# Kernel optimization log

Hardware: AMD Instinct MI355X
Metric: run time of the kernel (lower is better)

## Reference

```python
import jax, jax.numpy as jnp
import numpy as np

N = 100000   # nodes
DEG = 16     # fixed neighbor count per node
F_IN = 128
F_OUT = 32
H = 4        # heads


def setup_inputs() -> dict:
    key = jax.random.key(0)
    k1, k2, k3, k4 = jax.random.split(key, 4)
    x = jax.random.normal(k1, (N, F_IN), dtype=jnp.float32)
    neigh_idx = jax.random.randint(k2, (N, DEG), 0, N)
    # small scale keeps exp(leaky_relu(score)) well-conditioned (original exp's pre-softmax)
    Ws = jax.random.normal(k3, (H, F_OUT, F_IN), dtype=jnp.float32) * 0.05
    As = jax.random.normal(k4, (H, 2 * F_OUT, 1), dtype=jnp.float32) * 0.05
    return {"x": x, "neigh_idx": neigh_idx, "Ws": Ws, "As": As}


def reference(x, neigh_idx, Ws, As):
    n, _ = x.shape
    h, f_out, _ = Ws.shape
    # transformed node features per head: [H, N, F_out]
    t = jnp.einsum('hoi,ni->hno', Ws, x)
    # score a^T [Wh_src; Wh_dst] decomposes into src + dst dot products
    a = As[..., 0]                      # [H, 2*F_out]
    a_src, a_dst = a[:, :f_out], a[:, f_out:]
    s_src = jnp.einsum('hno,ho->hn', t, a_src)   # [H, N]
    s_dst = jnp.einsum('hno,ho->hn', t, a_dst)   # [H, N]
    # self node goes first in the softmax, matching the original loop
    full_idx = jnp.concatenate([jnp.arange(n)[:, None], neigh_idx], axis=1)  # [N, DEG+1]
    scores = s_src[:, :, None] + s_dst[:, full_idx]                           # [H, N, DEG+1]
    # faithful to original: exp(leaky_relu(.)) THEN softmax (double exponential)
    e = jnp.exp(jax.nn.leaky_relu(scores, 0.2))
    alphas = jax.nn.softmax(e, axis=-1)
    feats = t[:, full_idx]                                                    # [H, N, DEG+1, F_out]
    out = jnp.einsum('hnd,hndf->hnf', alphas, feats)                          # [H, N, F_out]
    # activation 'elu' -> heads concatenated: [N, H*F_out]
    out = jnp.transpose(out, (1, 0, 2)).reshape(n, h * f_out)
    return jax.nn.elu(out)
```

## Files before the change

### kernel.cpp

```cpp
#include <hip/hip_runtime.h>
#include <hip/hip_fp16.h>
#include <math.h>

#define NN 100000
#define DEG 16
#define F_IN 128
#define F_OUT 32
#define NH 4
#define FTOT 128

typedef _Float16 f16x8 __attribute__((ext_vector_type(8)));
typedef float f32x4 __attribute__((ext_vector_type(4)));

__device__ __forceinline__ int swz(int row, int col) {
    return row * 128 + (col ^ ((row & 7) << 3));
}

__global__ __launch_bounds__(256) void k0_wprep(
    const float* __restrict__ W,
    __half* __restrict__ W16) {
    const int g = blockIdx.x * 256 + threadIdx.x;
    const int row = g >> 4;
    const int col = (g & 15) * 8;
    const float4 v0 = *(const float4*)(W + row * F_IN + col);
    const float4 v1 = *(const float4*)(W + row * F_IN + col + 4);
    union { __half2 h2[4]; float4 f; } u;
    u.h2[0] = __float22half2_rn(make_float2(v0.x, v0.y));
    u.h2[1] = __float22half2_rn(make_float2(v0.z, v0.w));
    u.h2[2] = __float22half2_rn(make_float2(v1.x, v1.y));
    u.h2[3] = __float22half2_rn(make_float2(v1.z, v1.w));
    *(float4*)&W16[swz(row, col)] = u.f;
}

__global__ __launch_bounds__(256) void k1_proj(
    const float* __restrict__ x,
    const __half* __restrict__ W16,
    const float* __restrict__ As,
    __half* __restrict__ t,
    float* __restrict__ ssrc,
    float* __restrict__ sdst) {
    __shared__ __half xs[64 * 128];
    __shared__ __half wsh[128 * 128];

    const int tid = threadIdx.x;
    const int base = blockIdx.x * 64;

    {
        const int row = tid >> 2;
        const int q = tid & 3;
        int ng = base + row;
        if (ng >= NN) ng = NN - 1;
        const float* src = x + (long)ng * F_IN + q * 32;
#pragma unroll
        for (int i = 0; i < 4; ++i) {
            const float4 v0 = *(const float4*)(src + i * 8);
            const float4 v1 = *(const float4*)(src + i * 8 + 4);
            union { __half2 h2[4]; float4 f; } u;
            u.h2[0] = __float22half2_rn(make_float2(v0.x, v0.y));
            u.h2[1] = __float22half2_rn(make_float2(v0.z, v0.w));
            u.h2[2] = __float22half2_rn(make_float2(v1.x, v1.y));
            u.h2[3] = __float22half2_rn(make_float2(v1.z, v1.w));
            *(float4*)&xs[swz(row, q * 32 + i * 8)] = u.f;
        }
    }
    {
        const float4* src = (const float4*)W16;
        float4* dst = (float4*)wsh;
#pragma unroll
        for (int i = 0; i < 8; ++i) dst[tid + 256 * i] = src[tid + 256 * i];
    }
    __syncthreads();

    const int lane = tid & 63;
    const int wv = tid >> 6;
    const int mb = wv * 16;
    const int lr = lane & 15;
    const int lg = lane >> 4;

    f16x8 afr[4];
#pragma unroll
    for (int kk = 0; kk < 4; ++kk)
        afr[kk] = *(const f16x8*)&xs[swz(mb + lr, kk * 32 + lg * 8)];

    f32x4 acc[8];
#pragma unroll
    for (int nt = 0; nt < 8; ++nt) {
        f32x4 c = {0.f, 0.f, 0.f, 0.f};
#pragma unroll
        for (int kk = 0; kk < 4; ++kk) {
            const f16x8 b =
                *(const f16x8*)&wsh[swz(nt * 16 + lr, kk * 32 + lg * 8)];
            c = __builtin_amdgcn_mfma_f32_16x16x32_f16(afr[kk], b, c, 0, 0, 0);
        }
        acc[nt] = c;
    }

    __half* tst = &xs[mb * 128];
#pragma unroll
    for (int nt = 0; nt < 8; ++nt) {
#pragma unroll
        for (int r = 0; r < 4; ++r) {
            const int node = lg * 4 + r;
            const int feat = nt * 16 + lr;
            tst[node * 128 + (feat ^ ((node & 7) << 3))] =
                __float2half_rn(acc[nt][r]);
        }
    }
#pragma unroll
    for (int r = 0; r < 4; ++r) {
        const int row = r * 4 + lg;
        const int n = base + mb + row;
        if (n < NN) {
            const float4 v =
                *(const float4*)&tst[row * 128 + ((lr * 8) ^ ((row & 7) << 3))];
            *(float4*)(t + (long)n * FTOT + lr * 8) = v;
        }
    }

#pragma unroll
    for (int h = 0; h < NH; ++h) {
        const float as0 = As[h * 64 + lr];
        const float as1 = As[h * 64 + 16 + lr];
        const float ad0 = As[h * 64 + 32 + lr];
        const float ad1 = As[h * 64 + 48 + lr];
#pragma unroll
        for (int r = 0; r < 4; ++r) {
            float ps = acc[2 * h][r] * as0 + acc[2 * h + 1][r] * as1;
            float pd = acc[2 * h][r] * ad0 + acc[2 * h + 1][r] * ad1;
            ps += __shfl_xor(ps, 1); ps += __shfl_xor(ps, 2);
            ps += __shfl_xor(ps, 4); ps += __shfl_xor(ps, 8);
            pd += __shfl_xor(pd, 1); pd += __shfl_xor(pd, 2);
            pd += __shfl_xor(pd, 4); pd += __shfl_xor(pd, 8);
            if (lr == 0) {
                const int n = base + mb + lg * 4 + r;
                if (n < NN) {
                    ssrc[(long)n * NH + h] = ps;
                    sdst[(long)n * NH + h] = pd;
                }
            }
        }
    }
}

__global__ __launch_bounds__(256) void k2_attn(
    const int* __restrict__ nidx,
    const __half* __restrict__ t,
    const float* __restrict__ ssrc,
    const float* __restrict__ sdst,
    float* __restrict__ out) {
    __shared__ float salpha[4][17][4];
    __shared__ int sidx[4][17];

    const int lane = threadIdx.x & 63;
    const int wv = threadIdx.x >> 6;
    const int n = blockIdx.x * 4 + wv;

    if (lane < 17) {
        sidx[wv][lane] =
            (lane == 0)
                ? n
                : __builtin_nontemporal_load(&nidx[(long)n * DEG + (lane - 1)]);
    }
    __syncthreads();

    unsigned int pre[17];
#pragma unroll
    for (int d = 0; d < 17; ++d) {
        pre[d] = *(const unsigned int*)(t + (long)sidx[wv][d] * FTOT + 2 * lane);
    }

    const int h = lane >> 4;
    const int j = lane & 15;
    const float ssv = ssrc[(long)n * NH + h];

    float e_a;
    {
        float c = ssv + sdst[(long)sidx[wv][j] * NH + h];
        c = fmaxf(c, 0.f) + 0.2f * fminf(c, 0.f);
        e_a = expf(c);
    }
    float e_b = -INFINITY;
    if (j == 15) {
        float c = ssv + sdst[(long)sidx[wv][16] * NH + h];
        c = fmaxf(c, 0.f) + 0.2f * fminf(c, 0.f);
        e_b = expf(c);
    }

    float m = fmaxf(e_a, e_b);
#pragma unroll
    for (int mask = 8; mask >= 1; mask >>= 1)
        m = fmaxf(m, __shfl_xor(m, mask));

    const float pa = expf(e_a - m);
    const float pb = (j == 15) ? expf(e_b - m) : 0.f;
    float s = pa + pb;
#pragma unroll
    for (int mask = 8; mask >= 1; mask >>= 1)
        s += __shfl_xor(s, mask);

    const float inv = 1.0f / s;
    salpha[wv][j][h] = pa * inv;
    if (j == 15) salpha[wv][16][h] = pb * inv;
    __syncthreads();

    const int hc = lane >> 4;
    float ax = 0.f, ay = 0.f;
#pragma unroll
    for (int d = 0; d < 17; ++d) {
        const float a = salpha[wv][d][hc];
        const float2 f = __half22float2(*(const __half2*)&pre[d]);
        ax += a * f.x;
        ay += a * f.y;
    }

    const float yx = ax > 0.f ? ax : expm1f(ax);
    const float yy = ay > 0.f ? ay : expm1f(ay);
    union { float2 f2; double d; } o;
    o.f2 = make_float2(yx, yy);
    __builtin_nontemporal_store(o.d, (double*)(out + (long)n * FTOT + 2 * lane));
}

extern "C" void kernel_launch(void* const* d_in, const int* in_sizes, int n_in,
                              void* d_out, int out_size, void* d_ws, size_t ws_size,
                              hipStream_t stream) {
    const float* x = (const float*)d_in[0];
    const int* nidx = (const int*)d_in[1];
    const float* W = (const float*)d_in[2];
    const float* As = (const float*)d_in[3];
    float* out = (float*)d_out;

    __half* t = (__half*)d_ws;
    float* ssrc = (float*)((char*)d_ws + (size_t)NN * FTOT * sizeof(__half));
    float* sdst = ssrc + (size_t)NN * NH;
    __half* W16 = (__half*)(sdst + (size_t)NN * NH);

    k0_wprep<<<8, 256, 0, stream>>>(W, W16);
    k1_proj<<<(NN + 63) / 64, 256, 0, stream>>>(x, W16, As, t, ssrc, sdst);
    k2_attn<<<NN / 4, 256, 0, stream>>>(nidx, t, ssrc, sdst, out);
}
```

Baseline: 188.0 us.

## Load x and W fragments directly from global memory into MFMA registers in projection

The projection kernel stops staging x and the 32KB half-precision W into shared memory. Each lane now loads its x fragment straight from global memory, converts it to half in registers, and reads W fragments directly from global (L1/L2-cached). This removes the block-wide barrier and the per-block shared copy of W, and cuts LDS use from 48KB to 16KB per block, which should allow more resident blocks. The tradeoff is repeated, uncoalesced-ish global reads of W through the caches in place of fast LDS reads.

```diff
diff --git a/kernel.cpp b/kernel.cpp
--- a/kernel.cpp
+++ b/kernel.cpp
@@ -11,10 +11,6 @@
 
 typedef _Float16 f16x8 __attribute__((ext_vector_type(8)));
 typedef float f32x4 __attribute__((ext_vector_type(4)));
-
-__device__ __forceinline__ int swz(int row, int col) {
-    return row * 128 + (col ^ ((row & 7) << 3));
-}
 
 __global__ __launch_bounds__(256) void k0_wprep(
     const float* __restrict__ W,
@@ -29,7 +25,7 @@
     u.h2[1] = __float22half2_rn(make_float2(v0.z, v0.w));
     u.h2[2] = __float22half2_rn(make_float2(v1.x, v1.y));
     u.h2[3] = __float22half2_rn(make_float2(v1.z, v1.w));
-    *(float4*)&W16[swz(row, col)] = u.f;
+    *(float4*)&W16[row * F_IN + col] = u.f;
 }
 
 __global__ __launch_bounds__(256) void k1_proj(
@@ -39,48 +35,32 @@
     __half* __restrict__ t,
     float* __restrict__ ssrc,
     float* __restrict__ sdst) {
-    __shared__ __half xs[64 * 128];
-    __shared__ __half wsh[128 * 128];
+    __shared__ __half tsh[4][16 * 128];
 
     const int tid = threadIdx.x;
-    const int base = blockIdx.x * 64;
-
-    {
-        const int row = tid >> 2;
-        const int q = tid & 3;
-        int ng = base + row;
-        if (ng >= NN) ng = NN - 1;
-        const float* src = x + (long)ng * F_IN + q * 32;
-#pragma unroll
-        for (int i = 0; i < 4; ++i) {
-            const float4 v0 = *(const float4*)(src + i * 8);
-            const float4 v1 = *(const float4*)(src + i * 8 + 4);
-            union { __half2 h2[4]; float4 f; } u;
-            u.h2[0] = __float22half2_rn(make_float2(v0.x, v0.y));
-            u.h2[1] = __float22half2_rn(make_float2(v0.z, v0.w));
-            u.h2[2] = __float22half2_rn(make_float2(v1.x, v1.y));
-            u.h2[3] = __float22half2_rn(make_float2(v1.z, v1.w));
-            *(float4*)&xs[swz(row, q * 32 + i * 8)] = u.f;
-        }
-    }
-    {
-        const float4* src = (const float4*)W16;
-        float4* dst = (float4*)wsh;
-#pragma unroll
-        for (int i = 0; i < 8; ++i) dst[tid + 256 * i] = src[tid + 256 * i];
-    }
-    __syncthreads();
-
     const int lane = tid & 63;
     const int wv = tid >> 6;
+    const int base = blockIdx.x * 64;
     const int mb = wv * 16;
     const int lr = lane & 15;
     const int lg = lane >> 4;
 
+    int ng = base + mb + lr;
+    if (ng >= NN) ng = NN - 1;
+    const float* xrow = x + (long)ng * F_IN;
+
     f16x8 afr[4];
 #pragma unroll
-    for (int kk = 0; kk < 4; ++kk)
-        afr[kk] = *(const f16x8*)&xs[swz(mb + lr, kk * 32 + lg * 8)];
+    for (int kk = 0; kk < 4; ++kk) {
+        const float4 v0 = *(const float4*)(xrow + kk * 32 + lg * 8);
+        const float4 v1 = *(const float4*)(xrow + kk * 32 + lg * 8 + 4);
+        union { __half2 h2[4]; f16x8 f; } u;
+        u.h2[0] = __float22half2_rn(make_float2(v0.x, v0.y));
+        u.h2[1] = __float22half2_rn(make_float2(v0.z, v0.w));
+        u.h2[2] = __float22half2_rn(make_float2(v1.x, v1.y));
+        u.h2[3] = __float22half2_rn(make_float2(v1.z, v1.w));
+        afr[kk] = u.f;
+    }
 
     f32x4 acc[8];
 #pragma unroll
@@ -89,13 +69,13 @@
 #pragma unroll
         for (int kk = 0; kk < 4; ++kk) {
             const f16x8 b =
-                *(const f16x8*)&wsh[swz(nt * 16 + lr, kk * 32 + lg * 8)];
+                *(const f16x8*)&W16[(nt * 16 + lr) * F_IN + kk * 32 + lg * 8];
             c = __builtin_amdgcn_mfma_f32_16x16x32_f16(afr[kk], b, c, 0, 0, 0);
         }
         acc[nt] = c;
     }
 
-    __half* tst = &xs[mb * 128];
+    __half* tst = tsh[wv];
 #pragma unroll
     for (int nt = 0; nt < 8; ++nt) {
 #pragma unroll
```

Result: slower. 203.2 us (+8.1%).
